# Performance work log

Hardware: AMD Instinct MI355X
Metric: run time of the kernel (lower is better)

Reference implementation:

```python
import jax, jax.numpy as jnp
import numpy as np

S, N, F, E, H = 64, 1000, 64, 128, 2  # seq_len, nodes/graph, node_dim, emb_dim, heads
DEG = 8
C = E // H  # per-head channels


def setup_inputs() -> dict:
    key = jax.random.key(0)
    ks = jax.random.split(key, 16)
    Ntot = S * N
    Eg = N * DEG
    src = jax.random.randint(ks[0], (S, Eg), 0, N)
    dst = jax.random.randint(ks[1], (S, Eg), 0, N)
    off = (jnp.arange(S) * N)[:, None]
    edge_index = jnp.stack([(src + off).reshape(-1), (dst + off).reshape(-1)]).astype(jnp.int32)
    nfm = jax.random.normal(ks[2], (Ntot, F), jnp.float32)
    reachable = jax.random.uniform(ks[3], (S, N)) > 0.2
    reachable = reachable.at[:, 0].set(True)  # ensure each row has a reachable node
    h0 = jnp.zeros((N, E), jnp.float32)
    c0 = jnp.zeros((N, E), jnp.float32)

    def lin(k, i, o):
        return (jax.random.normal(k, (i, o), jnp.float32) / np.sqrt(i)).astype(jnp.float32)

    return dict(
        nfm=nfm, edge_index=edge_index, reachable=reachable, h0=h0, c0=c0,
        gat_W1=lin(ks[4], F, E), gat_b1=jnp.zeros((E,), jnp.float32),
        gat_att1=(jax.random.normal(ks[5], (H, C), jnp.float32) / np.sqrt(C)).astype(jnp.float32),
        gat_bias1=jnp.zeros((E,), jnp.float32),
        gat_W=(jax.random.normal(ks[6], (4, E, E), jnp.float32) / np.sqrt(E)).astype(jnp.float32),
        gat_b=jnp.zeros((4, E), jnp.float32),
        gat_att=(jax.random.normal(ks[7], (4, H, C), jnp.float32) / np.sqrt(C)).astype(jnp.float32),
        gat_bias=jnp.zeros((4, E), jnp.float32),
        lstm_Wih=(jax.random.normal(ks[8], (4 * E, E), jnp.float32) / np.sqrt(E)).astype(jnp.float32),
        lstm_Whh=(jax.random.normal(ks[9], (4 * E, E), jnp.float32) / np.sqrt(E)).astype(jnp.float32),
        lstm_bih=jnp.zeros((4 * E,), jnp.float32), lstm_bhh=jnp.zeros((4 * E,), jnp.float32),
        th6_W=lin(ks[10], E, E), th6_b=jnp.zeros((E,), jnp.float32),
        th7_W=lin(ks[11], E, E), th7_b=jnp.zeros((E,), jnp.float32),
        th5_W=lin(ks[12], 2 * E, 1), th5_b=jnp.zeros((1,), jnp.float32),
    )


def _gat_layer(x, src, dst, W, b, att, bias, Ntot):
    # GATv2Conv, share_weights=True: x_l == x_r = lin(x)
    Hh, Ch = att.shape
    xl = (x @ W + b).reshape(-1, Hh, Ch)                 # [Ntot,H,C]
    e = jax.nn.leaky_relu(xl[src] + xl[dst], 0.2)        # [Etot,H,C]
    logit = jnp.einsum('ehc,hc->eh', e, att)             # [Etot,H]
    m = jax.ops.segment_max(logit, dst, num_segments=Ntot)
    a = jnp.exp(logit - m[dst])                          # segment-stable softmax
    denom = jax.ops.segment_sum(a, dst, num_segments=Ntot)
    alpha = a / denom[dst]
    out = jax.ops.segment_sum(xl[src] * alpha[:, :, None], dst, num_segments=Ntot)
    return out.reshape(-1, Hh * Ch) + bias               # concat heads + bias


def _forward(nfm, edge_index, reachable, h0, c0, gat_W1, gat_b1, gat_att1, gat_bias1,
             gat_W, gat_b, gat_att, gat_bias, lstm_Wih, lstm_Whh, lstm_bih, lstm_bhh,
             th6_W, th6_b, th7_W, th7_b, th5_W, th5_b):
    Ntot = nfm.shape[0]
    loops = jnp.arange(Ntot, dtype=edge_index.dtype)     # add_self_loops=True
    src = jnp.concatenate([edge_index[0], loops])
    dst = jnp.concatenate([edge_index[1], loops])

    x = jax.nn.relu(_gat_layer(nfm, src, dst, gat_W1, gat_b1, gat_att1, gat_bias1, Ntot))
    for i in range(4):  # layers 2..5; no activation after last
        x = _gat_layer(x, src, dst, gat_W[i], gat_b[i], gat_att[i], gat_bias[i], Ntot)
        if i < 3:
            x = jax.nn.relu(x)

    mu = x.reshape(S, N, E)                              # [seq, batch(=nodes), emb]

    def step(carry, xt):
        h, c = carry
        g = xt @ lstm_Wih.T + lstm_bih + h @ lstm_Whh.T + lstm_bhh
        i_, f_, gg, o_ = jnp.split(g, 4, axis=-1)        # torch gate order i,f,g,o
        c = jax.nn.sigmoid(f_) * c + jax.nn.sigmoid(i_) * jnp.tanh(gg)
        h = jax.nn.sigmoid(o_) * jnp.tanh(c)
        return (h, c), h

    (hT, cT), mu = jax.lax.scan(step, (h0, c0), mu)      # mu: [S,N,E]

    meanpool = mu.mean(axis=1, keepdims=True)            # [S,1,E]
    gs = meanpool @ th6_W + th6_b
    la = mu @ th7_W + th7_b
    rep = jax.nn.relu(jnp.concatenate([jnp.broadcast_to(gs, la.shape), la], axis=-1))
    logits = (rep @ th5_W)[..., 0] + th5_b               # [S,N]
    logits = jnp.where(reachable, logits, -jnp.inf)
    prob = jax.nn.softmax(logits, axis=1)
    return prob, hT, cT


def reference(nfm, edge_index, reachable, h0, c0, gat_W1, gat_b1, gat_att1, gat_bias1,
              gat_W, gat_b, gat_att, gat_bias, lstm_Wih, lstm_Whh, lstm_bih, lstm_bhh,
              th6_W, th6_b, th7_W, th7_b, th5_W, th5_b):
    return _forward(nfm, edge_index, reachable, h0, c0, gat_W1, gat_b1, gat_att1, gat_bias1,
                    gat_W, gat_b, gat_att, gat_bias, lstm_Wih, lstm_Whh, lstm_bih, lstm_bhh,
                    th6_W, th6_b, th7_W, th7_b, th5_W, th5_b)
```

## Files before the change

### kernel.cpp

```cpp
#include <hip/hip_runtime.h>
#include <hip/hip_bf16.h>

#define SQ   64
#define NN   1000
#define NT   64000
#define EE   128
#define EG   512000
#define ET   576000

#define WS_XA      0ull
#define WS_XB      33000000ull
#define WS_ROWPTR  66000000ull
#define WS_CURSOR  66300000ull
#define WS_SRCS    66600000ull
#define WS_INCL    69000000ull
#define WS_BSUM    69300000ull
#define WS_BOFF    69302048ull
#define WS_MODE    69304096ull
#define WS_WQA     70000000ull
#define WS_WQB     70262144ull
#define WS_AS      70600000ull
#define WS_LOGIT2  70700000ull
#define WS2_XC     33000000ull
#define WS2_BFRAG  164100000ull
#define WS2_GHI    164300000ull
#define WS2_GLO    164650000ull
#define WS2_B512   165000000ull
#define WS2_MODE   165010000ull
#define WS2_AS     165020000ull
#define WS2_LOGIT2 165100000ull
#define WS2_NEED   165360000ull
#define G_W1    0
#define G_WL    8192
#define G_PROJ  73728
#define G_W7    139264

typedef __attribute__((ext_vector_type(8))) short short8;
typedef __attribute__((ext_vector_type(4))) float f32x4;

__device__ __forceinline__ float rdlane(float v, int l) {
    return __int_as_float(__builtin_amdgcn_readlane(__float_as_int(v), l));
}
__device__ __forceinline__ float sigm(float x) { return 1.0f / (1.0f + __expf(-x)); }
__device__ __forceinline__ float tanh_f(float x) {
    x = fminf(fmaxf(x, -30.0f), 30.0f);
    float e = __expf(2.0f * x);
    return (e - 1.0f) / (e + 1.0f);
}
__device__ __forceinline__ float tanh2(float x) {
    return 2.0f / (1.0f + __expf(-2.0f * x)) - 1.0f;
}
__device__ __forceinline__ ushort f2bf(float x) {
    unsigned u = __float_as_uint(x);
    unsigned r = (u + 0x7FFFu + ((u >> 16) & 1u)) >> 16;
    return (ushort)r;
}
__device__ __forceinline__ float bf2f(ushort h) {
    return __uint_as_float(((unsigned)h) << 16);
}

__global__ void detect_mode_k(const unsigned char* __restrict__ p, int* __restrict__ mode) {
    __shared__ int f0, f3;
    const int t = threadIdx.x;
    if (t == 0) { f0 = 0; f3 = 0; }
    __syncthreads();
    int l0 = 0, l3 = 0;
    for (int i = t; i < 16000; i += 256) {
        if (p[4 * i])     l0 = 1;
        if (p[4 * i + 3]) l3 = 1;
    }
    if (l0) atomicOr(&f0, 1);
    if (l3) atomicOr(&f3, 1);
    __syncthreads();
    if (t == 0) {
        int m;
        if (f0 && f3)      m = 1;
        else if (f0)       m = 0;
        else               m = 2;
        *mode = m;
    }
}

__global__ void zero_ints_k(int* __restrict__ p, int n) {
    int i = blockIdx.x * 256 + threadIdx.x;
    if (i < n) p[i] = 0;
}
__global__ void hist_k(const int* __restrict__ ei, int* __restrict__ deg) {
    int e = blockIdx.x * 256 + threadIdx.x;
    if (e < ET) {
        int d = (e < EG) ? ei[EG + e] : (e - EG);
        atomicAdd(deg + d, 1);
    }
}
__global__ void scan1_k(const int* __restrict__ deg, int* __restrict__ incl, int* __restrict__ bsum) {
    __shared__ int sh[256];
    const int t = threadIdx.x;
    const int i = blockIdx.x * 256 + t;
    sh[t] = deg[i];
    __syncthreads();
    for (int o = 1; o < 256; o <<= 1) {
        int add = (t >= o) ? sh[t - o] : 0;
        __syncthreads();
        sh[t] += add;
        __syncthreads();
    }
    incl[i] = sh[t];
    if (t == 255) bsum[blockIdx.x] = sh[255];
}
__global__ void scan2_k(const int* __restrict__ bsum, int* __restrict__ boff) {
    __shared__ int sh[256];
    const int t = threadIdx.x;
    int v = (t < 250) ? bsum[t] : 0;
    sh[t] = v;
    __syncthreads();
    for (int o = 1; o < 256; o <<= 1) {
        int add = (t >= o) ? sh[t - o] : 0;
        __syncthreads();
        sh[t] += add;
        __syncthreads();
    }
    if (t < 250) boff[t] = sh[t] - v;
}
__global__ void scan3_k(const int* __restrict__ incl, const int* __restrict__ boff,
                        int* __restrict__ rowptr, int* __restrict__ cursor_deg) {
    const int i = blockIdx.x * 256 + threadIdx.x;
    int total = incl[i] + boff[blockIdx.x];
    int excl  = total - cursor_deg[i];
    rowptr[i] = excl;
    cursor_deg[i] = excl;
    if (i == NT - 1) rowptr[NT] = total;
}
__global__ void fill_k(const int* __restrict__ ei, int* __restrict__ cursor, int* __restrict__ srcs) {
    int e = blockIdx.x * 256 + threadIdx.x;
    if (e < ET) {
        int s_, d_;
        if (e < EG) { s_ = ei[e]; d_ = ei[EG + e]; }
        else        { s_ = e - EG; d_ = s_; }
        int p = atomicAdd(cursor + d_, 1);
        srcs[p] = s_;
    }
}

__global__ void build_gfrag_k(const float* __restrict__ src, const int ks, const int ns,
                              const int K, ushort* __restrict__ dhi, ushort* __restrict__ dlo,
                              const int total) {
    int id = blockIdx.x * 256 + threadIdx.x;
    if (id < total) {
        int j = id & 7, lane = (id >> 3) & 63;
        int f = id >> 9;
        int KT = K >> 5;
        int nt = f / KT, kt = f - nt * KT;
        int n = nt * 16 + (lane & 15);
        int k = kt * 32 + ((lane >> 4) << 3) + j;
        float v = src[(size_t)k * ks + (size_t)n * ns];
        ushort h = f2bf(v);
        dhi[id] = h;
        dlo[id] = f2bf(v - bf2f(h));
    }
}
__global__ void bias512_k(const float* __restrict__ bih, const float* __restrict__ bhh,
                          float* __restrict__ b512) {
    int i = blockIdx.x * 256 + threadIdx.x;
    if (i < 512) b512[i] = bih[i] + bhh[i];
}

template <int KT>
__global__ __launch_bounds__(256) void gemm_mf(
    const float* __restrict__ x, const ushort* __restrict__ bhi,
    const ushort* __restrict__ blo, const float* __restrict__ bias,
    float* __restrict__ out, const int ldout)
{
    constexpr int K = KT * 32;
    __shared__ __align__(16) ushort ahi_s[64 * 136];
    __shared__ __align__(16) ushort alo_s[64 * 136];
    const int t = threadIdx.x;
    const int w = t >> 6, lane = t & 63;
    const int quad = lane >> 4, col = lane & 15;
    const int row0 = blockIdx.x * 64;
    const int col0 = blockIdx.y * 128;

    {
        const int r  = t >> 2;
        const int kc = (t & 3) * (K / 4);
        const float* xr = x + (size_t)(row0 + r) * K + kc;
        ushort* dh = ahi_s + r * 136 + kc;
        ushort* dl = alo_s + r * 136 + kc;
#pragma unroll
        for (int k = 0; k < K / 4; k += 4) {
            float4 v = *(const float4*)(xr + k);
            ushort h0_ = f2bf(v.x), h1_ = f2bf(v.y), h2_ = f2bf(v.z), h3_ = f2bf(v.w);
            ushort l0_ = f2bf(v.x - bf2f(h0_)), l1_ = f2bf(v.y - bf2f(h1_));
            ushort l2_ = f2bf(v.z - bf2f(h2_)), l3_ = f2bf(v.w - bf2f(h3_));
            *(uint2*)(dh + k) = make_uint2((uint)h0_ | ((uint)h1_ << 16),
                                           (uint)h2_ | ((uint)h3_ << 16));
            *(uint2*)(dl + k) = make_uint2((uint)l0_ | ((uint)l1_ << 16),
                                           (uint)l2_ | ((uint)l3_ << 16));
        }
    }
    __syncthreads();

    short8 ah[KT], al[KT];
#pragma unroll
    for (int kt = 0; kt < KT; kt++) {
        const int off = (w * 16 + col) * 136 + kt * 32 + quad * 8;
        ah[kt] = *(const short8*)(ahi_s + off);
        al[kt] = *(const short8*)(alo_s + off);
    }

    f32x4 acc[8];
#pragma unroll
    for (int q = 0; q < 8; q++) acc[q] = (f32x4){0.f, 0.f, 0.f, 0.f};

#pragma unroll
    for (int q = 0; q < 8; q++) {
#pragma unroll
        for (int kt = 0; kt < KT; kt++) {
            const int f = ((((col0 >> 4) + q) * KT + kt) * 64 + lane) * 8;
            short8 bh = *(const short8*)(bhi + f);
            short8 bl = *(const short8*)(blo + f);
            acc[q] = __builtin_amdgcn_mfma_f32_16x16x32_bf16(ah[kt], bh, acc[q], 0, 0, 0);
            acc[q] = __builtin_amdgcn_mfma_f32_16x16x32_bf16(al[kt], bh, acc[q], 0, 0, 0);
            acc[q] = __builtin_amdgcn_mfma_f32_16x16x32_bf16(ah[kt], bl, acc[q], 0, 0, 0);
        }
    }

#pragma unroll
    for (int q = 0; q < 8; q++) {
        float bv = bias[col0 + q * 16 + col];
#pragma unroll
        for (int r = 0; r < 4; r++) {
            out[(size_t)(row0 + w * 16 + quad * 4 + r) * ldout + col0 + q * 16 + col]
                = acc[q][r] + bv;
        }
    }
}

template <int K>
__global__ __launch_bounds__(256) void gemm3(
    const float* __restrict__ x, const float* __restrict__ W,
    const float* __restrict__ b, float* __restrict__ out)
{
    __shared__ float Wsh[64 * 128];
    __shared__ float xT[64][132];
    const int t = threadIdx.x;
    const int row0 = blockIdx.x * 128;
    const int cg = t & 15;
    const int rg = t >> 4;
    float4 acc[8][2];
#pragma unroll
    for (int r = 0; r < 8; r++) {
        acc[r][0] = make_float4(0.f, 0.f, 0.f, 0.f);
        acc[r][1] = make_float4(0.f, 0.f, 0.f, 0.f);
    }
    for (int k0 = 0; k0 < K; k0 += 64) {
        for (int i = t * 4; i < 64 * 128; i += 1024)
            *(float4*)(Wsh + i) = *(const float4*)(W + (size_t)k0 * 128 + i);
        for (int i = t * 4; i < 128 * 64; i += 1024) {
            int r = i >> 6, k = i & 63;
            float4 v = *(const float4*)(x + (size_t)(row0 + r) * K + k0 + k);
            xT[k + 0][r] = v.x; xT[k + 1][r] = v.y;
            xT[k + 2][r] = v.z; xT[k + 3][r] = v.w;
        }
        __syncthreads();
#pragma unroll 2
        for (int k = 0; k < 64; k++) {
            float4 w0 = *(const float4*)(Wsh + k * 128 + cg * 8);
            float4 w1 = *(const float4*)(Wsh + k * 128 + cg * 8 + 4);
            float4 x0 = *(const float4*)(&xT[k][rg * 8]);
            float4 x1 = *(const float4*)(&xT[k][rg * 8 + 4]);
            float xv[8] = {x0.x, x0.y, x0.z, x0.w, x1.x, x1.y, x1.z, x1.w};
#pragma unroll
            for (int r = 0; r < 8; r++) {
                acc[r][0].x += xv[r] * w0.x; acc[r][0].y += xv[r] * w0.y;
                acc[r][0].z += xv[r] * w0.z; acc[r][0].w += xv[r] * w0.w;
                acc[r][1].x += xv[r] * w1.x; acc[r][1].y += xv[r] * w1.y;
                acc[r][1].z += xv[r] * w1.z; acc[r][1].w += xv[r] * w1.w;
            }
        }
        __syncthreads();
    }
    float4 bv0 = *(const float4*)(b + cg * 8);
    float4 bv1 = *(const float4*)(b + cg * 8 + 4);
#pragma unroll
    for (int r = 0; r < 8; r++) {
        float4 o0, o1;
        o0.x = acc[r][0].x + bv0.x; o0.y = acc[r][0].y + bv0.y;
        o0.z = acc[r][0].z + bv0.z; o0.w = acc[r][0].w + bv0.w;
        o1.x = acc[r][1].x + bv1.x; o1.y = acc[r][1].y + bv1.y;
        o1.z = acc[r][1].z + bv1.z; o1.w = acc[r][1].w + bv1.w;
        float* op = out + (size_t)(row0 + rg * 8 + r) * 128 + cg * 8;
        *(float4*)(op) = o0;
        *(float4*)(op + 4) = o1;
    }
}

__global__ __launch_bounds__(256) void gat_fused_k(
    const float* __restrict__ xl, const int* __restrict__ rowptr,
    const int* __restrict__ srcs, const float* __restrict__ att,
    const float* __restrict__ bias, float* __restrict__ out, const int do_relu)
{
    const int lane = threadIdx.x & 63;
    const int q = lane & 31;
    const int h = lane >> 5;
    const int b = blockIdx.x;
    const int g = b & 7;
    const int j = b >> 3;
    const int jq = j / 250;
    const int jj = j - jq * 250;
    const int s = g + 8 * jq;
    const int n = s * NN + jj * 4 + (threadIdx.x >> 6);

    const float4 a4 = *(const float4*)(att + q * 4);
    const float4 xd = *(const float4*)(xl + (size_t)n * 128 + q * 4);
    const int i0 = rowptr[n], i1 = rowptr[n + 1];

    float m = -1e30f, d = 0.f;
    float ax = 0.f, ay = 0.f, az = 0.f, aw = 0.f;

    for (int base = i0, i = i0 + h; base < i1; base += 2, i += 2) {
        const bool valid = (i < i1);
        int sv = 0;
        if (valid) sv = srcs[i];
        const float4 xs = *(const float4*)(xl + (size_t)sv * 128 + q * 4);
        float u0 = xs.x + xd.x, u1 = xs.y + xd.y;
        float u2 = xs.z + xd.z, u3 = xs.w + xd.w;
        float p;
        p  = a4.x * fmaxf(u0, 0.2f * u0);
        p += a4.y * fmaxf(u1, 0.2f * u1);
        p += a4.z * fmaxf(u2, 0.2f * u2);
        p += a4.w * fmaxf(u3, 0.2f * u3);
        p += __shfl_xor(p, 1);
        p += __shfl_xor(p, 2);
        p += __shfl_xor(p, 4);
        p += __shfl_xor(p, 8);
        float mn = fmaxf(m, valid ? p : -1e30f);
        float sc = __expf(m - mn);
        float wgt = valid ? __expf(p - mn) : 0.f;
        d  = d  * sc + wgt;
        ax = ax * sc + wgt * xs.x;
        ay = ay * sc + wgt * xs.y;
        az = az * sc + wgt * xs.z;
        aw = aw * sc + wgt * xs.w;
        m = mn;
    }

    float m2 = __shfl_xor(m, 32);
    float d2 = __shfl_xor(d, 32);
    float bx = __shfl_xor(ax, 32);
    float by = __shfl_xor(ay, 32);
    float bz = __shfl_xor(az, 32);
    float bw = __shfl_xor(aw, 32);
    float mm = fmaxf(m, m2);
    float s1 = __expf(m - mm), s2 = __expf(m2 - mm);
    float den = d * s1 + d2 * s2;
    float inv = 1.f / den;
    float4 bv = *(const float4*)(bias + q * 4);
    float ox = (ax * s1 + bx * s2) * inv + bv.x;
    float oy = (ay * s1 + by * s2) * inv + bv.y;
    float oz = (az * s1 + bz * s2) * inv + bv.z;
    float ow = (aw * s1 + bw * s2) * inv + bv.w;
    if (do_relu) {
        ox = fmaxf(ox, 0.f); oy = fmaxf(oy, 0.f);
        oz = fmaxf(oz, 0.f); ow = fmaxf(ow, 0.f);
    }
    if (lane < 32)
        *(float4*)(out + (size_t)n * 128 + q * 4) = make_float4(ox, oy, oz, ow);
}

__global__ void build_wq_k(const float* __restrict__ Wih, const float* __restrict__ Whh,
                           float4* __restrict__ WQa, float4* __restrict__ WQb) {
    int id = blockIdx.x * 256 + threadIdx.x;
    if (id < 64 * 256) {
        int kp = id >> 8, t = id & 255;
        int j1 = t, j2 = t + 256;
        WQa[id] = make_float4(Wih[(size_t)j1 * 128 + 2 * kp], Whh[(size_t)j1 * 128 + 2 * kp],
                              Wih[(size_t)j1 * 128 + 2 * kp + 1], Whh[(size_t)j1 * 128 + 2 * kp + 1]);
        WQb[id] = make_float4(Wih[(size_t)j2 * 128 + 2 * kp], Whh[(size_t)j2 * 128 + 2 * kp],
                              Wih[(size_t)j2 * 128 + 2 * kp + 1], Whh[(size_t)j2 * 128 + 2 * kp + 1]);
    }
}

__global__ void build_bfrag_k(const float* __restrict__ Whh, ushort* __restrict__ Bfrag) {
    int id = blockIdx.x * 256 + threadIdx.x;
    if (id < 65536) {
        int j = id & 7, lane = (id >> 3) & 63, kt = (id >> 9) & 3, tile = id >> 11;
        int gate = tile * 16 + (lane & 15);
        int k = kt * 32 + ((lane >> 4) << 3) + j;
        Bfrag[id] = f2bf(Whh[(size_t)gate * 128 + k]);
    }
}

#define LSTM_GROUP(buf, gbase)                                                     \
    _Pragma("unroll")                                                              \
    for (int i_ = 0; i_ < 4; i_++) {                                               \
        const int kp_ = (gbase) * 4 + i_;                                          \
        const float4 qa_ = buf[i_];                                                \
        const float4 qb_ = buf[4 + i_];                                            \
        _Pragma("unroll")                                                          \
        for (int n_ = 0; n_ < 4; n_++) {                                           \
            const float sx0_ = rdlane(xr[n_].x, kp_);                              \
            const float sh0_ = rdlane(hr[n_].x, kp_);                              \
            const float sx1_ = rdlane(xr[n_].y, kp_);                              \
            const float sh1_ = rdlane(hr[n_].y, kp_);                              \
            acc1[n_] += sx0_ * qa_.x + sh0_ * qa_.y + sx1_ * qa_.z + sh1_ * qa_.w; \
            acc2[n_] += sx0_ * qb_.x + sh0_ * qb_.y + sx1_ * qb_.z + sh1_ * qb_.w; \
        }                                                                          \
    }

__global__ __launch_bounds__(256, 1) void lstm_k(
    float* __restrict__ mu, const float4* __restrict__ WQa, const float4* __restrict__ WQb,
    const float* __restrict__ bih, const float* __restrict__ bhh,
    const float* __restrict__ h0, const float* __restrict__ c0,
    float* __restrict__ hT, float* __restrict__ cT)
{
    const int t = threadIdx.x, lane = t & 63;
    const int n0 = blockIdx.x * 4;
    __shared__ float hsh[4][128];
    __shared__ float gsh[4][512];
    const float b1 = bih[t] + bhh[t];
    const float b2 = bih[t + 256] + bhh[t + 256];
    float creg[2];
#pragma unroll
    for (int q = 0; q < 2; q++) {
        int id = t + 256 * q;
        creg[q] = c0[(size_t)(n0 + (id >> 7)) * 128 + (id & 127)];
    }
    for (int i = t; i < 512; i += 256)
        hsh[i >> 7][i & 127] = h0[(size_t)(n0 + (i >> 7)) * 128 + (i & 127)];

    const float4* pA = WQa + t;
    const float4* pB = WQb + t;

    float2 xr[4], xnx[4];
#pragma unroll
    for (int n = 0; n < 4; n++)
        xr[n] = *(const float2*)(mu + (size_t)n0 * 128 + n * 128 + lane * 2);
    __syncthreads();

    for (int s = 0; s < SQ; s++) {
        float* xrow = mu + ((size_t)s * NN + n0) * 128;
        float2 hr[4];
#pragma unroll
        for (int n = 0; n < 4; n++) hr[n] = *(const float2*)(&hsh[n][lane * 2]);

        float4 bufA[8], bufB[8];
#pragma unroll
        for (int i = 0; i < 4; i++) { bufA[i] = pA[i * 256]; bufA[4 + i] = pB[i * 256]; }

        if (s + 1 < SQ) {
            const float* xrow2 = mu + ((size_t)(s + 1) * NN + n0) * 128;
#pragma unroll
            for (int n = 0; n < 4; n++) xnx[n] = *(const float2*)(xrow2 + n * 128 + lane * 2);
        }

        float acc1[4], acc2[4];
#pragma unroll
        for (int n = 0; n < 4; n++) { acc1[n] = b1; acc2[n] = b2; }

        for (int g = 0; g < 16; g += 2) {
#pragma unroll
            for (int i = 0; i < 4; i++) {
                bufB[i]     = pA[((g + 1) * 4 + i) * 256];
                bufB[4 + i] = pB[((g + 1) * 4 + i) * 256];
            }
            LSTM_GROUP(bufA, g)
            if (g < 14) {
#pragma unroll
                for (int i = 0; i < 4; i++) {
                    bufA[i]     = pA[((g + 2) * 4 + i) * 256];
                    bufA[4 + i] = pB[((g + 2) * 4 + i) * 256];
                }
            }
            LSTM_GROUP(bufB, g + 1)
        }

#pragma unroll
        for (int n = 0; n < 4; n++) { gsh[n][t] = acc1[n]; gsh[n][t + 256] = acc2[n]; }
        __syncthreads();
#pragma unroll
        for (int q = 0; q < 2; q++) {
            int id = t + 256 * q;
            int n = id >> 7, e = id & 127;
            float iv = gsh[n][e], fv = gsh[n][128 + e];
            float gv = gsh[n][256 + e], ov = gsh[n][384 + e];
            float c = sigm(fv) * creg[q] + sigm(iv) * tanh_f(gv);
            float h = sigm(ov) * tanh_f(c);
            creg[q] = c;
            hsh[n][e] = h;
            xrow[n * 128 + e] = h;
            if (s == SQ - 1) {
                hT[(size_t)(n0 + n) * 128 + e] = h;
                cT[(size_t)(n0 + n) * 128 + e] = c;
            }
        }
#pragma unroll
        for (int n = 0; n < 4; n++) xr[n] = xnx[n];
        __syncthreads();
    }
}

__global__ __launch_bounds__(512, 2) void lstm9_k(
    float* __restrict__ mu, const float* __restrict__ xC,
    const ushort* __restrict__ Bfrag,
    const float* __restrict__ h0, const float* __restrict__ c0,
    float* __restrict__ hT, float* __restrict__ cT)
{
    const int t = threadIdx.x;
    const int w = t >> 6, lane = t & 63;
    const int quad = lane >> 4, col = lane & 15;
    const int n0 = blockIdx.x * 2;
    const int enode = (t >> 7) & 1;
    const int ech   = t & 127;
    const bool epi  = (t < 256);

    __shared__ __align__(16) ushort hbuf[2][2][16 * 136];
    __shared__ float gsh[2][512];

    short8 bf[4][4];
#pragma unroll
    for (int g4 = 0; g4 < 4; g4++)
#pragma unroll
        for (int kt = 0; kt < 4; kt++) {
            int tile = g4 * 8 + w;
            bf[g4][kt] = *(const short8*)(Bfrag + (((tile * 4 + kt) * 64 + lane) << 3));
        }

    for (int i = t; i < 2048; i += 512) {
        int node = i >> 7, ee = i & 127;
        float v = (node < 2) ? h0[(size_t)(n0 + node) * 128 + ee] : 0.f;
        ushort hh = f2bf(v), hl = f2bf(v - bf2f(hh));
        hbuf[0][0][node * 136 + ee] = hh; hbuf[0][1][node * 136 + ee] = hl;
        hbuf[1][0][node * 136 + ee] = hh; hbuf[1][1][node * 136 + ee] = hl;
    }
    float cst = 0.f;
    float xcr[4], xcn[4];
    if (epi) {
        cst = c0[(size_t)(n0 + enode) * 128 + ech];
#pragma unroll
        for (int g4 = 0; g4 < 4; g4++)
            xcr[g4] = xC[((size_t)(n0 + enode)) * 512 + g4 * 128 + ech];
    }
    __syncthreads();

    int p = 0;
    for (int s = 0; s < SQ; s++) {
        if (epi && s + 1 < SQ) {
            const float* xn = xC + ((size_t)(s + 1) * NN + n0 + enode) * 512;
#pragma unroll
            for (int g4 = 0; g4 < 4; g4++)
                xcn[g4] = xn[g4 * 128 + ech];
        }

        short8 ahi[4], alo[4];
#pragma unroll
        for (int kt = 0; kt < 4; kt++) {
            ahi[kt] = *(const short8*)(&hbuf[p][0][col * 136 + kt * 32 + quad * 8]);
            alo[kt] = *(const short8*)(&hbuf[p][1][col * 136 + kt * 32 + quad * 8]);
        }

        f32x4 acc[4];
#pragma unroll
        for (int g4 = 0; g4 < 4; g4++) acc[g4] = (f32x4){0.f, 0.f, 0.f, 0.f};
#pragma unroll
        for (int kt = 0; kt < 4; kt++) {
#pragma unroll
            for (int g4 = 0; g4 < 4; g4++)
                acc[g4] = __builtin_amdgcn_mfma_f32_16x16x32_bf16(ahi[kt], bf[g4][kt], acc[g4], 0, 0, 0);
#pragma unroll
            for (int g4 = 0; g4 < 4; g4++)
                acc[g4] = __builtin_amdgcn_mfma_f32_16x16x32_bf16(alo[kt], bf[g4][kt], acc[g4], 0, 0, 0);
        }

        if (quad == 0) {
#pragma unroll
            for (int g4 = 0; g4 < 4; g4++)
#pragma unroll
                for (int r = 0; r < 2; r++)
                    gsh[r][(g4 * 8 + w) * 16 + col] = acc[g4][r];
        }
        __syncthreads();

        if (epi) {
            float iv = gsh[enode][0 * 128 + ech] + xcr[0];
            float fv = gsh[enode][1 * 128 + ech] + xcr[1];
            float gv = gsh[enode][2 * 128 + ech] + xcr[2];
            float ov = gsh[enode][3 * 128 + ech] + xcr[3];
            float c = sigm(fv) * cst + sigm(iv) * tanh2(gv);
            float h = sigm(ov) * tanh2(c);
            cst = c;
            const int pn = p ^ 1;
            ushort hh = f2bf(h);
            hbuf[pn][0][enode * 136 + ech] = hh;
            hbuf[pn][1][enode * 136 + ech] = f2bf(h - bf2f(hh));
            mu[((size_t)s * NN + n0 + enode) * 128 + ech] = h;
            if (s == SQ - 1) {
                hT[(size_t)(n0 + enode) * 128 + ech] = h;
                cT[(size_t)(n0 + enode) * 128 + ech] = c;
            }
#pragma unroll
            for (int g4 = 0; g4 < 4; g4++) xcr[g4] = xcn[g4];
        }
        p ^= 1;
        __syncthreads();
    }
}

__global__ __launch_bounds__(256) void meanpool_gs_k(
    const float* __restrict__ mu, const float* __restrict__ W6,
    const float* __restrict__ b6, const float* __restrict__ w5,
    float* __restrict__ A)
{
    const int s = blockIdx.x, t = threadIdx.x;
    const int ch = t & 127, half = t >> 7;
    __shared__ float mp[128];
    __shared__ float red[256];
    float acc = 0.f;
    for (int n = half * 500; n < (half + 1) * 500; n++)
        acc += mu[((size_t)s * NN + n) * 128 + ch];
    red[t] = acc;
    __syncthreads();
    if (t < 128) mp[t] = (red[t] + red[t + 128]) * 0.001f;
    __syncthreads();
    float g = 0.f;
    if (t < 128) {
        g = b6[t];
        for (int k = 0; k < 128; k++) g += mp[k] * W6[(size_t)k * 128 + t];
        g = fmaxf(g, 0.f) * w5[t];
    }
    red[t] = g;
    __syncthreads();
    for (int o = 128; o > 0; o >>= 1) {
        if (t < o) red[t] += red[t + o];
        __syncthreads();
    }
    if (t == 0) A[s] = red[0];
}

__global__ __launch_bounds__(256) void rowdot_k(
    const float* __restrict__ la, const float* __restrict__ w5,
    const float* __restrict__ b5, const float* __restrict__ A,
    float* __restrict__ out)
{
    const int lane = threadIdx.x & 63;
    const int row = blockIdx.x * 4 + (threadIdx.x >> 6);
    float2 v = *(const float2*)(la + (size_t)row * 128 + lane * 2);
    float2 w = *(const float2*)(w5 + 128 + lane * 2);
    float x = fmaxf(v.x, 0.f) * w.x + fmaxf(v.y, 0.f) * w.y;
#pragma unroll
    for (int o = 32; o; o >>= 1) x += __shfl_down(x, o);
    if (lane == 0) out[row] = x + A[row / NN] + b5[0];
}

__device__ __forceinline__ bool reach_at(const void* reach, int mode, int idx) {
    if (mode == 0) return ((const int*)reach)[idx] != 0;
    if (mode == 1) return ((const unsigned char*)reach)[idx] != 0;
    return ((const float*)reach)[idx] != 0.f;
}
__global__ __launch_bounds__(256) void softmax_k(
    const float* __restrict__ lg, const void* __restrict__ reach,
    const int* __restrict__ mode, float* __restrict__ prob)
{
    const int s = blockIdx.x, t = threadIdx.x;
    const int m = *mode;
    __shared__ float red[256];
    float mx = -1e30f;
    for (int i = t; i < NN; i += 256) {
        int idx = s * NN + i;
        if (reach_at(reach, m, idx)) mx = fmaxf(mx, lg[idx]);
    }
    red[t] = mx;
    __syncthreads();
    for (int o = 128; o; o >>= 1) {
        if (t < o) red[t] = fmaxf(red[t], red[t + o]);
        __syncthreads();
    }
    mx = red[0];
    __syncthreads();
    float sum = 0.f;
    for (int i = t; i < NN; i += 256) {
        int idx = s * NN + i;
        float v = reach_at(reach, m, idx) ? __expf(lg[idx] - mx) : 0.f;
        prob[idx] = v;
        sum += v;
    }
    red[t] = sum;
    __syncthreads();
    for (int o = 128; o; o >>= 1) {
        if (t < o) red[t] += red[t + o];
        __syncthreads();
    }
    float inv = 1.f / red[0];
    for (int i = t; i < NN; i += 256) prob[s * NN + i] *= inv;
}

extern "C" void kernel_launch(void* const* d_in, const int* in_sizes, int n_in,
                              void* d_out, int out_size, void* d_ws, size_t ws_size,
                              hipStream_t stream) {
    const float* nfm   = (const float*)d_in[0];
    const int*   ei    = (const int*)d_in[1];
    const void*  reach = d_in[2];
    const float* h0    = (const float*)d_in[3];
    const float* c0    = (const float*)d_in[4];
    const float* W1    = (const float*)d_in[5];
    const float* b1    = (const float*)d_in[6];
    const float* att1  = (const float*)d_in[7];
    const float* bias1 = (const float*)d_in[8];
    const float* Wl    = (const float*)d_in[9];
    const float* bl    = (const float*)d_in[10];
    const float* attl  = (const float*)d_in[11];
    const float* biasl = (const float*)d_in[12];
    const float* Wih   = (const float*)d_in[13];
    const float* Whh   = (const float*)d_in[14];
    const float* bih   = (const float*)d_in[15];
    const float* bhh   = (const float*)d_in[16];
    const float* W6    = (const float*)d_in[17];
    const float* b6    = (const float*)d_in[18];
    const float* W7    = (const float*)d_in[19];
    const float* b7    = (const float*)d_in[20];
    const float* w5    = (const float*)d_in[21];
    const float* b5    = (const float*)d_in[22];

    char* ws = (char*)d_ws;
    const bool bigws = (ws_size >= WS2_NEED);

    float*  xA     = (float*)(ws + WS_XA);
    float*  xB     = (float*)(ws + WS_XB);
    int*    rowptr = (int*)(ws + WS_ROWPTR);
    int*    cursor = (int*)(ws + WS_CURSOR);
    int*    srcs   = (int*)(ws + WS_SRCS);
    int*    incl   = (int*)(ws + WS_INCL);
    int*    bsum   = (int*)(ws + WS_BSUM);
    int*    boff   = (int*)(ws + WS_BOFF);
    int*    modep  = bigws ? (int*)(ws + WS2_MODE)     : (int*)(ws + WS_MODE);
    float*  As     = bigws ? (float*)(ws + WS2_AS)     : (float*)(ws + WS_AS);
    float*  logit2 = bigws ? (float*)(ws + WS2_LOGIT2) : (float*)(ws + WS_LOGIT2);
    float*  xC     = (float*)(ws + WS2_XC);
    ushort* Bfrag  = (ushort*)(ws + WS2_BFRAG);
    ushort* ghi    = (ushort*)(ws + WS2_GHI);
    ushort* glo    = (ushort*)(ws + WS2_GLO);
    float*  b512   = (float*)(ws + WS2_B512);
    float4* WQa    = (float4*)(ws + WS_WQA);
    float4* WQb    = (float4*)(ws + WS_WQB);

    float* prob = (float*)d_out;
    float* hT   = (float*)d_out + 64000;
    float* cT   = (float*)d_out + 192000;

    detect_mode_k<<<1, 256, 0, stream>>>((const unsigned char*)reach, modep);
    zero_ints_k<<<250, 256, 0, stream>>>(cursor, NT);
    hist_k<<<2250, 256, 0, stream>>>(ei, cursor);
    scan1_k<<<250, 256, 0, stream>>>(cursor, incl, bsum);
    scan2_k<<<1, 256, 0, stream>>>(bsum, boff);
    scan3_k<<<250, 256, 0, stream>>>(incl, boff, rowptr, cursor);
    fill_k<<<2250, 256, 0, stream>>>(ei, cursor, srcs);
    if (bigws) {
        build_bfrag_k<<<256, 256, 0, stream>>>(Whh, Bfrag);
        bias512_k<<<2, 256, 0, stream>>>(bih, bhh, b512);
        build_gfrag_k<<<32, 256, 0, stream>>>(W1, 128, 1, 64, ghi + G_W1, glo + G_W1, 8192);
        for (int i = 0; i < 4; i++)
            build_gfrag_k<<<64, 256, 0, stream>>>(Wl + (size_t)i * 16384, 128, 1, 128,
                                                  ghi + G_WL + i * 16384, glo + G_WL + i * 16384, 16384);
        build_gfrag_k<<<256, 256, 0, stream>>>(Wih, 1, 128, 128, ghi + G_PROJ, glo + G_PROJ, 65536);
        build_gfrag_k<<<64, 256, 0, stream>>>(W7, 128, 1, 128, ghi + G_W7, glo + G_W7, 16384);
    } else {
        build_wq_k<<<64, 256, 0, stream>>>(Wih, Whh, WQa, WQb);
    }

    for (int l = 0; l < 5; l++) {
        if (bigws) {
            if (l == 0)
                gemm_mf<2><<<dim3(1000, 1), 256, 0, stream>>>(nfm, ghi + G_W1, glo + G_W1, b1, xB, 128);
            else
                gemm_mf<4><<<dim3(1000, 1), 256, 0, stream>>>(xA, ghi + G_WL + (l - 1) * 16384,
                                                              glo + G_WL + (l - 1) * 16384,
                                                              bl + (l - 1) * 128, xB, 128);
        } else {
            if (l == 0)
                gemm3<64><<<500, 256, 0, stream>>>(nfm, W1, b1, xB);
            else
                gemm3<128><<<500, 256, 0, stream>>>(xA, Wl + (size_t)(l - 1) * 128 * 128,
                                                    bl + (l - 1) * 128, xB);
        }
        const float* att  = (l == 0) ? att1  : attl  + (l - 1) * 128;
        const float* bias = (l == 0) ? bias1 : biasl + (l - 1) * 128;
        gat_fused_k<<<16000, 256, 0, stream>>>(xB, rowptr, srcs, att, bias, xA,
                                               (l < 4) ? 1 : 0);
    }

    if (bigws) {
        gemm_mf<4><<<dim3(1000, 4), 256, 0, stream>>>(xA, ghi + G_PROJ, glo + G_PROJ, b512, xC, 512);
        lstm9_k<<<500, 512, 0, stream>>>(xA, xC, Bfrag, h0, c0, hT, cT);
    } else {
        lstm_k<<<250, 256, 0, stream>>>(xA, WQa, WQb, bih, bhh, h0, c0, hT, cT);
    }

    meanpool_gs_k<<<64, 256, 0, stream>>>(xA, W6, b6, w5, As);
    if (bigws)
        gemm_mf<4><<<dim3(1000, 1), 256, 0, stream>>>(xA, ghi + G_W7, glo + G_W7, b7, xB, 128);
    else
        gemm3<128><<<500, 256, 0, stream>>>(xA, W7, b7, xB);
    rowdot_k<<<16000, 256, 0, stream>>>(xB, w5, b5, As, logit2);
    softmax_k<<<64, 256, 0, stream>>>(logit2, reach, modep, prob);
}
```

Measured before the change: 732.5 us.

## Use MFMA-fragment LDS layout, prefetch GAT edge indices, run four LSTM nodes per block

The GEMM A-tile in LDS is stored in MFMA fragment order, so each lane reads its short8 contiguously instead of through a padded row layout. The GAT aggregation loop now loads the next edge's source index one iteration ahead, hiding that dependent load. The LSTM recurrence kernel handles four nodes per block instead of two, using all 512 threads in the epilogue and halving the grid to 250 blocks. Fewer blocks on a long sequential recurrence may reduce parallelism across CUs.

```diff
diff --git a/kernel.cpp b/kernel.cpp
--- a/kernel.cpp
+++ b/kernel.cpp
@@ -171,8 +171,8 @@
     float* __restrict__ out, const int ldout)
 {
     constexpr int K = KT * 32;
-    __shared__ __align__(16) ushort ahi_s[64 * 136];
-    __shared__ __align__(16) ushort alo_s[64 * 136];
+    __shared__ __align__(16) ushort ahi_s[KT * 4 * 64 * 8];
+    __shared__ __align__(16) ushort alo_s[KT * 4 * 64 * 8];
     const int t = threadIdx.x;
     const int w = t >> 6, lane = t & 63;
     const int quad = lane >> 4, col = lane & 15;
@@ -182,19 +182,21 @@
     {
         const int r  = t >> 2;
         const int kc = (t & 3) * (K / 4);
+        const int rw = r >> 4, rcol = r & 15;
         const float* xr = x + (size_t)(row0 + r) * K + kc;
-        ushort* dh = ahi_s + r * 136 + kc;
-        ushort* dl = alo_s + r * 136 + kc;
 #pragma unroll
         for (int k = 0; k < K / 4; k += 4) {
+            const int ch = kc + k;
+            const int idx = (((ch >> 5) * 4 + rw) * 64 + ((ch >> 3) & 3) * 16 + rcol) * 8
+                            + (ch & 7);
             float4 v = *(const float4*)(xr + k);
             ushort h0_ = f2bf(v.x), h1_ = f2bf(v.y), h2_ = f2bf(v.z), h3_ = f2bf(v.w);
             ushort l0_ = f2bf(v.x - bf2f(h0_)), l1_ = f2bf(v.y - bf2f(h1_));
             ushort l2_ = f2bf(v.z - bf2f(h2_)), l3_ = f2bf(v.w - bf2f(h3_));
-            *(uint2*)(dh + k) = make_uint2((uint)h0_ | ((uint)h1_ << 16),
-                                           (uint)h2_ | ((uint)h3_ << 16));
-            *(uint2*)(dl + k) = make_uint2((uint)l0_ | ((uint)l1_ << 16),
-                                           (uint)l2_ | ((uint)l3_ << 16));
+            *(uint2*)(ahi_s + idx) = make_uint2((uint)h0_ | ((uint)h1_ << 16),
+                                                (uint)h2_ | ((uint)h3_ << 16));
+            *(uint2*)(alo_s + idx) = make_uint2((uint)l0_ | ((uint)l1_ << 16),
+                                                (uint)l2_ | ((uint)l3_ << 16));
         }
     }
     __syncthreads();
@@ -202,7 +204,7 @@
     short8 ah[KT], al[KT];
 #pragma unroll
     for (int kt = 0; kt < KT; kt++) {
-        const int off = (w * 16 + col) * 136 + kt * 32 + quad * 8;
+        const int off = ((kt * 4 + w) * 64 + lane) * 8;
         ah[kt] = *(const short8*)(ahi_s + off);
         al[kt] = *(const short8*)(alo_s + off);
     }
@@ -317,10 +319,11 @@
     float m = -1e30f, d = 0.f;
     float ax = 0.f, ay = 0.f, az = 0.f, aw = 0.f;
 
-    for (int base = i0, i = i0 + h; base < i1; base += 2, i += 2) {
+    int i = i0 + h;
+    int sv = (i < i1) ? srcs[i] : 0;
+    for (int base = i0; base < i1; base += 2) {
         const bool valid = (i < i1);
-        int sv = 0;
-        if (valid) sv = srcs[i];
+        const int svn = (i + 2 < i1) ? srcs[i + 2] : 0;
         const float4 xs = *(const float4*)(xl + (size_t)sv * 128 + q * 4);
         float u0 = xs.x + xd.x, u1 = xs.y + xd.y;
         float u2 = xs.z + xd.z, u3 = xs.w + xd.w;
@@ -342,6 +345,8 @@
         az = az * sc + wgt * xs.z;
         aw = aw * sc + wgt * xs.w;
         m = mn;
+        sv = svn;
+        i += 2;
     }
 
     float m2 = __shfl_xor(m, 32);
@@ -499,7 +504,7 @@
     }
 }
 
-__global__ __launch_bounds__(512, 2) void lstm9_k(
+__global__ __launch_bounds__(512, 2) void lstm10_k(
     float* __restrict__ mu, const float* __restrict__ xC,
     const ushort* __restrict__ Bfrag,
     const float* __restrict__ h0, const float* __restrict__ c0,
@@ -507,14 +512,13 @@
 {
     const int t = threadIdx.x;
     const int w = t >> 6, lane = t & 63;
-    const int quad = lane >> 4, col = lane & 15;
-    const int n0 = blockIdx.x * 2;
-    const int enode = (t >> 7) & 1;
+    const int quad = lane >> 4;
+    const int n0 = blockIdx.x * 4;
+    const int enode = t >> 7;
     const int ech   = t & 127;
-    const bool epi  = (t < 256);
-
-    __shared__ __align__(16) ushort hbuf[2][2][16 * 136];
-    __shared__ float gsh[2][512];
+
+    __shared__ __align__(16) ushort hP[2][2][2048];
+    __shared__ float gsh[4][512];
 
     short8 bf[4][4];
 #pragma unroll
@@ -525,26 +529,28 @@
             bf[g4][kt] = *(const short8*)(Bfrag + (((tile * 4 + kt) * 64 + lane) << 3));
         }
 
-    for (int i = t; i < 2048; i += 512) {
-        int node = i >> 7, ee = i & 127;
-        float v = (node < 2) ? h0[(size_t)(n0 + node) * 128 + ee] : 0.f;
+    const int epkt = ech >> 5, epqd = (ech >> 3) & 3, epj = ech & 7;
+    const int epidx = epkt * 512 + (epqd * 16 + enode) * 8 + epj;
+
+    for (int i = t; i < 2 * 2 * 2048; i += 512) ((ushort*)hP)[i] = 0;
+    __syncthreads();
+    {
+        float v = h0[(size_t)(n0 + enode) * 128 + ech];
         ushort hh = f2bf(v), hl = f2bf(v - bf2f(hh));
-        hbuf[0][0][node * 136 + ee] = hh; hbuf[0][1][node * 136 + ee] = hl;
-        hbuf[1][0][node * 136 + ee] = hh; hbuf[1][1][node * 136 + ee] = hl;
-    }
-    float cst = 0.f;
+        hP[0][0][epidx] = hh; hP[0][1][epidx] = hl;
+        hP[1][0][epidx] = hh; hP[1][1][epidx] = hl;
+    }
+    float cst = c0[(size_t)(n0 + enode) * 128 + ech];
+
     float xcr[4], xcn[4];
-    if (epi) {
-        cst = c0[(size_t)(n0 + enode) * 128 + ech];
-#pragma unroll
-        for (int g4 = 0; g4 < 4; g4++)
-            xcr[g4] = xC[((size_t)(n0 + enode)) * 512 + g4 * 128 + ech];
-    }
+#pragma unroll
+    for (int g4 = 0; g4 < 4; g4++)
+        xcr[g4] = xC[((size_t)(n0 + enode)) * 512 + g4 * 128 + ech];
     __syncthreads();
 
     int p = 0;
     for (int s = 0; s < SQ; s++) {
-        if (epi && s + 1 < SQ) {
+        if (s + 1 < SQ) {
             const float* xn = xC + ((size_t)(s + 1) * NN + n0 + enode) * 512;
 #pragma unroll
             for (int g4 = 0; g4 < 4; g4++)
@@ -554,8 +560,8 @@
         short8 ahi[4], alo[4];
 #pragma unroll
         for (int kt = 0; kt < 4; kt++) {
-            ahi[kt] = *(const short8*)(&hbuf[p][0][col * 136 + kt * 32 + quad * 8]);
-            alo[kt] = *(const short8*)(&hbuf[p][1][col * 136 + kt * 32 + quad * 8]);
+            ahi[kt] = *(const short8*)(&hP[p][0][kt * 512 + lane * 8]);
+            alo[kt] = *(const short8*)(&hP[p][1][kt * 512 + lane * 8]);
         }
 
         f32x4 acc[4];
@@ -572,15 +578,16 @@
         }
 
         if (quad == 0) {
+            const int col = lane & 15;
 #pragma unroll
             for (int g4 = 0; g4 < 4; g4++)
 #pragma unroll
-                for (int r = 0; r < 2; r++)
+                for (int r = 0; r < 4; r++)
                     gsh[r][(g4 * 8 + w) * 16 + col] = acc[g4][r];
         }
         __syncthreads();
 
-        if (epi) {
+        {
             float iv = gsh[enode][0 * 128 + ech] + xcr[0];
             float fv = gsh[enode][1 * 128 + ech] + xcr[1];
             float gv = gsh[enode][2 * 128 + ech] + xcr[2];
@@ -590,17 +597,17 @@
             cst = c;
             const int pn = p ^ 1;
             ushort hh = f2bf(h);
-            hbuf[pn][0][enode * 136 + ech] = hh;
-            hbuf[pn][1][enode * 136 + ech] = f2bf(h - bf2f(hh));
+            hP[pn][0][epidx] = hh;
+            hP[pn][1][epidx] = f2bf(h - bf2f(hh));
             mu[((size_t)s * NN + n0 + enode) * 128 + ech] = h;
             if (s == SQ - 1) {
                 hT[(size_t)(n0 + enode) * 128 + ech] = h;
                 cT[(size_t)(n0 + enode) * 128 + ech] = c;
             }
-#pragma unroll
-            for (int g4 = 0; g4 < 4; g4++) xcr[g4] = xcn[g4];
-        }
-        p ^= 1;
+            p = pn;
+        }
+#pragma unroll
+        for (int g4 = 0; g4 < 4; g4++) xcr[g4] = xcn[g4];
         __syncthreads();
     }
 }
@@ -789,7 +796,7 @@
 
     if (bigws) {
         gemm_mf<4><<<dim3(1000, 4), 256, 0, stream>>>(xA, ghi + G_PROJ, glo + G_PROJ, b512, xC, 512);
-        lstm9_k<<<500, 512, 0, stream>>>(xA, xC, Bfrag, h0, c0, hT, cT);
+        lstm10_k<<<250, 512, 0, stream>>>(xA, xC, Bfrag, h0, c0, hT, cT);
     } else {
         lstm_k<<<250, 256, 0, stream>>>(xA, WQa, WQb, bih, bhh, h0, c0, hT, cT);
     }
```

Measured after the change: 692.9 us. -5.4%, faster.
